# Kernel optimization log

Hardware: AMD Instinct MI355X
Metric: run time of the kernel (lower is better)

The kernel has to match this reference:

```python
import jax, jax.numpy as jnp
import numpy as np

B, P, V = 8, 16, 32
N_TH1 = 20
N_TH2 = 2 * (N_TH1 - 1) + 1
NPC, NNS, NOUT = 16384, 8192, 8192


def make_directions(n_th1):
    n_th2 = 2 * (n_th1 - 1) + 1
    th1 = np.linspace(-np.pi / 2, np.pi / 2, n_th1)
    th2 = np.linspace(-np.pi, np.pi, n_th2)
    c1, s1 = np.cos(th1), np.sin(th1)
    c2, s2 = np.cos(th2), np.sin(th2)
    ds = []
    for i in range(1, n_th1 - 1):
        for j in range(n_th2 - 1):
            ds.append([c1[i] * c2[j], c1[i] * s2[j], s1[i]])
    ds.append([c1[0] * c2[0], c1[0] * s2[0], s1[0]])
    ds.append([c1[-1] * c2[0], c1[-1] * s2[0], s1[-1]])
    return np.asarray(ds, np.float32)

DIRS = jnp.asarray(make_directions(N_TH1))
D = DIRS.shape[0]  # (n_th1-2)*(n_th2-1)+2 = 686


def _spt(dirs, verts, smooth, trans):
    # dirs [B,P,N,3], verts [B,P,V,3] (centered), trans [B,P,1,3]
    z = jnp.einsum('bpvc,bpnc->bpvn', verts, dirs)          # [B,P,V,N]
    zm = jnp.maximum(z, 0.0)
    pe = smooth[:, :, None, None]                            # [B,P,1,1]
    maxz = jnp.clip(jnp.max(z, axis=2, keepdims=True), 1e-30, 1e30)
    k = 1.0 / maxz                                           # [B,P,1,N]
    zmk = jnp.clip(zm * k, 1e-30, 1e30)                      # tiny floor keeps pow grads finite
    sum_zm_p = jnp.sum(zmk ** pe, axis=2, keepdims=True)     # [B,P,1,N]
    h = sum_zm_p ** (1.0 / pe)                               # normalized support value
    s = jnp.clip(h, 1e-30, 1e30)
    dhdz = jnp.clip((zmk / s) ** (pe - 1.0), 1e-30, 1e30)    # [B,P,V,N]
    surf = jnp.einsum('bpvn,bpvc->bpnc', dhdz, verts) + trans
    h_out = jnp.clip(h / k, -1e30, 1e30).transpose(0, 1, 3, 2)  # [B,P,N,1]
    return h_out, surf


def _distance(verts, smooth, trans, pts, normal_filter=None):
    # pts [B,P,N,3]: per-part query points in global coords
    local = pts - trans
    nrm = jnp.sqrt(jnp.clip(jnp.sum(local * local, -1, keepdims=True), 1e-40, 1e40))
    d = local / nrm                                          # unit directions [B,P,N,3]
    h, surf = _spt(d, verts, smooth, trans)
    dist = nrm - h                                           # signed distance to support plane
    if normal_filter is not None:
        dist = jnp.where(normal_filter, 100.0, dist)
    return dist, surf, d


def _overlap(verts, smooth, trans):
    t = trans[:, :, 0, :]                                    # [B,P,3]
    diff = t[:, None, :, :] - t[:, :, None, :]               # [B,i,j,3] = t_j - t_i
    dn = jnp.sqrt(jnp.clip(jnp.sum(diff * diff, -1, keepdims=True), 1e-20, 1e20))
    eyem = jnp.eye(t.shape[1], dtype=t.dtype)[None, :, :, None]
    safe = jnp.array([1.0, 0.0, 0.0], dtype=t.dtype)
    d = diff / dn * (1.0 - eyem) + eyem * safe               # safe diagonal direction
    h, _ = _spt(d, verts, smooth, trans)                     # [B,P,P,1] support of part i toward j
    sep = dn - h - jnp.swapaxes(h, 1, 2)                     # center gap minus both supports
    return jax.nn.relu(-sep) * (1.0 - eyem)


def _forward(vertices, smoothness, pointcloud, nearsurf, out):
    mean_v = jnp.mean(vertices, axis=2, keepdims=True)       # [B,P,1,3]
    local_v = vertices - mean_v
    x = jnp.broadcast_to(DIRS[None, None], (B, P, D, 3))
    h, _ = _spt(x, local_v, smoothness, mean_v)              # [B,P,D,1]
    overlap = _overlap(local_v, smoothness, mean_v)
    pc = jnp.broadcast_to(pointcloud[:, None], (B, P, NPC, 3))
    distance, _, _ = _distance(local_v, smoothness, mean_v, pc)
    scale = jnp.clip(jnp.max(h, axis=2, keepdims=True), 1e-10, 10.0)  # [B,P,1,1]
    _, surf_pts, normals = _distance(local_v, smoothness, mean_v, x * scale + mean_v)
    surf_points = surf_pts.reshape(B, P * D, 3)
    sp2 = jnp.broadcast_to(surf_points[:, None], (B, P, P * D, 3))
    local_trans = jnp.transpose(mean_v, (0, 2, 1, 3)) - mean_v        # [B,P,P,3]
    nf = jnp.einsum('bijc,bidc->bijd', local_trans, normals)          # [B,P,P,D]
    normal_filter = nf.reshape(B, P, P * D)[..., None] < 0
    surf_distance, _, _ = _distance(local_v, smoothness, mean_v, sp2, normal_filter=normal_filter)
    sd = surf_distance.reshape(B, P, P, D, 1)
    df = 100.0 * jnp.eye(P, dtype=sd.dtype)[None, :, :, None, None]
    sd = jnp.where(df > 0, df, sd)                           # mask self-distance
    surf_distance = sd.reshape(B, P, P * D, 1)
    ns = jnp.broadcast_to(nearsurf[:, None], (B, P, NNS, 3))
    nearsurf_dist, _, _ = _distance(local_v, smoothness, mean_v, ns)
    op = jnp.broadcast_to(out[:, None], (B, P, NOUT, 3))
    out_dist, _, _ = _distance(local_v, smoothness, mean_v, op)
    return overlap, distance, x, surf_distance, surf_points, nearsurf_dist, out_dist


def setup_inputs() -> dict:
    key = jax.random.key(0)
    k1, k2, k3, k4, k5, k6 = jax.random.split(key, 6)
    centers = jax.random.uniform(k1, (B, P, 1, 3), minval=-1.0, maxval=1.0)
    vertices = centers + 0.3 * jax.random.normal(k2, (B, P, V, 3))
    smoothness = 2.5 + 7.5 * jax.random.uniform(k3, (B, P))
    pointcloud = jax.random.uniform(k4, (B, NPC, 3), minval=-1.5, maxval=1.5)
    nearsurf = jax.random.uniform(k5, (B, NNS, 3), minval=-1.5, maxval=1.5)
    out = jax.random.uniform(k6, (B, NOUT, 3), minval=-2.0, maxval=2.0)
    return {"vertices": vertices, "smoothness": smoothness, "pointcloud": pointcloud,
            "nearsurf": nearsurf, "out": out}


def reference(vertices, smoothness, pointcloud, nearsurf, out):
    return _forward(vertices, smoothness, pointcloud, nearsurf, out)
```

## Files before the change

kernel.cpp:

```cpp
#include <hip/hip_runtime.h>
#include <math.h>

#define PP 16
#define VV 32
#define DD 686

__device__ __forceinline__ float clampf(float x, float lo, float hi) {
    return fminf(fmaxf(x, lo), hi);
}
__device__ __forceinline__ double clampd(double x, double lo, double hi) {
    return fmin(fmax(x, lo), hi);
}
__device__ __forceinline__ float fexp2(float x) { return __builtin_amdgcn_exp2f(x); }
__device__ __forceinline__ float flog2(float x) { return __builtin_amdgcn_logf(x); }
__device__ __forceinline__ float frcp (float x) { return __builtin_amdgcn_rcpf(x); }
__device__ __forceinline__ float frsq (float x) { return __builtin_amdgcn_rsqf(x); }

__device__ __forceinline__ float spt_support_f(const float* __restrict__ sv, float pe, float inv_pe,
                                               float dx, float dy, float dz)
{
    float z[VV];
    float maxz = -1e38f;
#pragma unroll
    for (int k = 0; k < VV; ++k) {
        float zz = sv[3*k+0]*dx + sv[3*k+1]*dy + sv[3*k+2]*dz;
        z[k] = zz;
        maxz = fmaxf(maxz, zz);
    }
    maxz = clampf(maxz, 1e-30f, 1e30f);
    float kk = frcp(maxz);
    float sum = 0.0f;
#pragma unroll
    for (int k = 0; k < VV; ++k) {
        float zm = clampf(fmaxf(z[k], 0.0f) * kk, 1e-30f, 1e30f);
        sum += fexp2(pe * flog2(zm));
    }
    float h = fexp2(flog2(sum) * inv_pe);
    return clampf(h * maxz, -1e30f, 1e30f);
}

__global__ void k_dirs(float* __restrict__ dirs)
{
    int idx = blockIdx.x * blockDim.x + threadIdx.x;
    if (idx >= DD) return;
    int i, j;
    if (idx < 684)      { i = idx / 38 + 1; j = idx - (idx / 38) * 38; }
    else if (idx == 684){ i = 0;  j = 0; }
    else                { i = 19; j = 0; }
    const double pi = 3.14159265358979323846;
    double th1 = -pi * 0.5 + (double)i * (pi / 19.0);
    double th2 = -pi       + (double)j * (pi / 19.0);
    dirs[3*idx+0] = (float)(cos(th1) * cos(th2));
    dirs[3*idx+1] = (float)(cos(th1) * sin(th2));
    dirs[3*idx+2] = (float)(sin(th1));
}

__global__ void k_prep(const float* __restrict__ verts, const float* __restrict__ smooth,
                       double* __restrict__ dmean, float* __restrict__ fmean,
                       float* __restrict__ flocal, float* __restrict__ fpe,
                       float* __restrict__ finvpe, int BP)
{
    int bp = blockIdx.x * blockDim.x + threadIdx.x;
    if (bp >= BP) return;
    const float* vv = verts + (size_t)bp * VV * 3;
    double sx = 0.0, sy = 0.0, sz = 0.0;
#pragma unroll
    for (int k = 0; k < VV; ++k) {
        sx += (double)vv[3*k+0];
        sy += (double)vv[3*k+1];
        sz += (double)vv[3*k+2];
    }
    double mx = sx / 32.0, my = sy / 32.0, mz = sz / 32.0;
    dmean[3*bp+0] = mx; dmean[3*bp+1] = my; dmean[3*bp+2] = mz;
    fmean[3*bp+0] = (float)mx; fmean[3*bp+1] = (float)my; fmean[3*bp+2] = (float)mz;
    float* lv = flocal + (size_t)bp * VV * 3;
#pragma unroll
    for (int k = 0; k < VV; ++k) {
        lv[3*k+0] = (float)((double)vv[3*k+0] - mx);
        lv[3*k+1] = (float)((double)vv[3*k+1] - my);
        lv[3*k+2] = (float)((double)vv[3*k+2] - mz);
    }
    float pe = smooth[bp];
    fpe[bp] = pe;
    finvpe[bp] = 1.0f / pe;
}

__global__ void __launch_bounds__(256) k_scale_x(
        const float* __restrict__ dirs, const float* __restrict__ flocal,
        const float* __restrict__ fpe, const float* __restrict__ finvpe,
        double* __restrict__ dscale, float* __restrict__ fscale,
        float* __restrict__ out2)
{
    int bp = blockIdx.x;
    __shared__ float sv[VV*3];
    __shared__ float red[4];
    int tid = threadIdx.x;
    if (tid < VV*3) sv[tid] = flocal[(size_t)bp*VV*3 + tid];
    __syncthreads();
    float pe = fpe[bp], ipe = finvpe[bp];
    float m = -1e38f;
    for (int dd = tid; dd < DD; dd += 256) {
        float dxf = dirs[3*dd+0], dyf = dirs[3*dd+1], dzf = dirs[3*dd+2];
        float hs = spt_support_f(sv, pe, ipe, dxf, dyf, dzf);
        m = fmaxf(m, hs);
        float* xp = out2 + ((size_t)bp * DD + dd) * 3;
        xp[0] = dxf; xp[1] = dyf; xp[2] = dzf;
    }
#pragma unroll
    for (int o = 32; o > 0; o >>= 1) m = fmaxf(m, __shfl_down(m, o));
    if ((tid & 63) == 0) red[tid >> 6] = m;
    __syncthreads();
    if (tid == 0) {
        m = fmaxf(fmaxf(red[0], red[1]), fmaxf(red[2], red[3]));
        m = clampf(m, 1e-10f, 10.0f);
        fscale[bp] = m;
        dscale[bp] = (double)m;
    }
}

__global__ void __launch_bounds__(256) k_surfpts(
        const float* __restrict__ dirs, const float* __restrict__ flocal,
        const float* __restrict__ fmean, const float* __restrict__ fpe,
        const float* __restrict__ finvpe, const float* __restrict__ fscale,
        float* __restrict__ fsurf, float* __restrict__ out4)
{
    int bp = blockIdx.x;
    __shared__ float sv[VV*3];
    int tid = threadIdx.x;
    if (tid < VV*3) sv[tid] = flocal[(size_t)bp*VV*3 + tid];
    __syncthreads();
    float pe = fpe[bp], ipe = finvpe[bp];
    float sc = fscale[bp];
    float m0 = fmean[3*bp+0], m1 = fmean[3*bp+1], m2 = fmean[3*bp+2];
    for (int dd = tid; dd < DD; dd += 256) {
        float xd = dirs[3*dd+0], yd = dirs[3*dd+1], zd = dirs[3*dd+2];
        float lx = (xd * sc + m0) - m0;
        float ly = (yd * sc + m1) - m1;
        float lz = (zd * sc + m2) - m2;
        float n2 = clampf(lx*lx + ly*ly + lz*lz, 1e-40f, 1e40f);
        float invr = frsq(n2);
        float dx = lx * invr, dy = ly * invr, dz = lz * invr;

        float l2z[VV];
        float maxz = -1e38f;
        float zz[VV];
#pragma unroll
        for (int k = 0; k < VV; ++k) {
            float z = sv[3*k+0]*dx + sv[3*k+1]*dy + sv[3*k+2]*dz;
            zz[k] = z;
            maxz = fmaxf(maxz, z);
        }
        maxz = clampf(maxz, 1e-30f, 1e30f);
        float kk = frcp(maxz);
        float sum = 0.0f;
#pragma unroll
        for (int k = 0; k < VV; ++k) {
            float zm = clampf(fmaxf(zz[k], 0.0f) * kk, 1e-30f, 1e30f);
            float l2 = flog2(zm);
            l2z[k] = l2;
            sum += fexp2(pe * l2);
        }
        float l2sum = flog2(sum);
        float h = fexp2(l2sum * ipe);
        float s = clampf(h, 1e-30f, 1e30f);
        float l2s = flog2(s);
        float pem1 = pe - 1.0f;
        float sxx = 0.f, syy = 0.f, szz2 = 0.f;
#pragma unroll
        for (int k = 0; k < VV; ++k) {
            float dh = clampf(fexp2(pem1 * (l2z[k] - l2s)), 1e-30f, 1e30f);
            sxx += dh * sv[3*k+0];
            syy += dh * sv[3*k+1];
            szz2 += dh * sv[3*k+2];
        }
        sxx += m0; syy += m1; szz2 += m2;
        float* spp = fsurf + ((size_t)bp * DD + dd) * 3;
        spp[0] = sxx; spp[1] = syy; spp[2] = szz2;
        float* op = out4 + ((size_t)bp * DD + dd) * 3;
        op[0] = sxx; op[1] = syy; op[2] = szz2;
    }
}

__global__ void __launch_bounds__(256) k_overlap(
        const float* __restrict__ flocal, const double* __restrict__ dmean,
        const float* __restrict__ fpe, const float* __restrict__ finvpe,
        float* __restrict__ out0)
{
    int b = blockIdx.x;
    __shared__ float  sv[PP*VV*3];
    __shared__ double smd[PP*3];
    __shared__ float  spe[PP];
    __shared__ float  sipe[PP];
    __shared__ float  sh[PP*PP];
    int tid = threadIdx.x;
    for (int t = tid; t < PP*VV*3; t += 256) sv[t] = flocal[(size_t)b*PP*VV*3 + t];
    if (tid < PP*3) smd[tid]  = dmean[(size_t)b*PP*3 + tid];
    if (tid < PP)  { spe[tid] = fpe[b*PP + tid]; sipe[tid] = finvpe[b*PP + tid]; }
    __syncthreads();
    int i = tid >> 4, j = tid & 15;
    double tx = smd[3*j+0] - smd[3*i+0];
    double ty = smd[3*j+1] - smd[3*i+1];
    double tz = smd[3*j+2] - smd[3*i+2];
    double dn2 = clampd(tx*tx + ty*ty + tz*tz, 1e-20, 1e20);
    double dn = sqrt(dn2);
    float dx, dy, dz;
    if (i == j) { dx = 1.0f; dy = 0.0f; dz = 0.0f; }
    else        { dx = (float)(tx/dn); dy = (float)(ty/dn); dz = (float)(tz/dn); }
    sh[tid] = spt_support_f(&sv[i*VV*3], spe[i], sipe[i], dx, dy, dz);
    __syncthreads();
    double sep = dn - (double)sh[i*16 + j] - (double)sh[j*16 + i];
    double ov = (i == j) ? 0.0 : fmax(-sep, 0.0);
    out0[(size_t)b*PP*PP + tid] = (float)ov;
}

__global__ void __launch_bounds__(256) k_dist(
        const float* __restrict__ pts, int N,
        const float* __restrict__ flocal, const float* __restrict__ fmean,
        const float* __restrict__ fpe, const float* __restrict__ finvpe,
        float* __restrict__ outp)
{
    int bp = blockIdx.x;
    int b  = bp >> 4;
    __shared__ float sv[VV*3];
    int tid = threadIdx.x;
    if (tid < VV*3) sv[tid] = flocal[(size_t)bp*VV*3 + tid];
    __syncthreads();
    float pe = fpe[bp], ipe = finvpe[bp];
    float m0 = fmean[3*bp+0], m1 = fmean[3*bp+1], m2 = fmean[3*bp+2];
    int n = blockIdx.y * 256 + tid;
    if (n >= N) return;
    const float* pp = pts + ((size_t)b * N + n) * 3;
    float lx = pp[0] - m0;
    float ly = pp[1] - m1;
    float lz = pp[2] - m2;
    float n2 = clampf(lx*lx + ly*ly + lz*lz, 1e-40f, 1e40f);
    float invr = frsq(n2);
    float nrm = n2 * invr;
    float dx = lx * invr, dy = ly * invr, dz = lz * invr;
    float hs = spt_support_f(sv, pe, ipe, dx, dy, dz);
    outp[(size_t)bp * N + n] = nrm - hs;
}

__global__ void __launch_bounds__(256) k_surfdist(
        const float* __restrict__ fsurf, const float* __restrict__ dirs,
        const float* __restrict__ flocal, const double* __restrict__ dmean,
        const float* __restrict__ fmean,
        const float* __restrict__ fpe, const float* __restrict__ finvpe,
        const double* __restrict__ dscale,
        float* __restrict__ out3)
{
    int bp = blockIdx.x;
    int b  = bp >> 4;
    int i  = bp & 15;
    __shared__ float sv[VV*3];
    int tid = threadIdx.x;
    if (tid < VV*3) sv[tid] = flocal[(size_t)bp*VV*3 + tid];
    __syncthreads();
    float pe = fpe[bp], ipe = finvpe[bp];
    double sc = dscale[bp];
    double mi0 = dmean[3*bp+0], mi1 = dmean[3*bp+1], mi2 = dmean[3*bp+2];
    int q = blockIdx.y * 256 + tid;
    if (q >= PP*DD) return;
    int j  = q / DD;
    int dd = q - j * DD;
    double xd = (double)dirs[3*dd+0], yd = (double)dirs[3*dd+1], zd = (double)dirs[3*dd+2];
    double nlx = (xd * sc + mi0) - mi0;
    double nly = (yd * sc + mi1) - mi1;
    double nlz = (zd * sc + mi2) - mi2;
    double nn2 = clampd(nlx*nlx + nly*nly + nlz*nlz, 1e-40, 1e40);
    double nnr = sqrt(nn2);
    const double* mj = dmean + (size_t)(b*PP + j) * 3;
    double tx = mj[0] - mi0, ty = mj[1] - mi1, tz = mj[2] - mi2;
    double nf = (tx*nlx + ty*nly + tz*nlz) / nnr;
    float dist;
    if (i == j || nf < 0.0) {
        dist = 100.0f;
    } else {
        float fm0 = fmean[3*bp+0], fm1 = fmean[3*bp+1], fm2 = fmean[3*bp+2];
        const float* sp = fsurf + ((size_t)b * PP * DD + q) * 3;
        float lx = sp[0] - fm0;
        float ly = sp[1] - fm1;
        float lz = sp[2] - fm2;
        float n2 = clampf(lx*lx + ly*ly + lz*lz, 1e-40f, 1e40f);
        float invr = frsq(n2);
        float nrm = n2 * invr;
        float dx = lx * invr, dy = ly * invr, dz = lz * invr;
        float hs = spt_support_f(sv, pe, ipe, dx, dy, dz);
        dist = nrm - hs;
    }
    out3[(size_t)bp * PP * DD + q] = dist;
}

extern "C" void kernel_launch(void* const* d_in, const int* in_sizes, int n_in,
                              void* d_out, int out_size, void* d_ws, size_t ws_size,
                              hipStream_t stream)
{
    const float* verts  = nullptr;
    const float* smooth = nullptr;
    const float* pcb    = nullptr;
    const float* nsb    = nullptr;
    const float* ob     = nullptr;
    const float* dirsin = nullptr;
    int Bv = 8, BP = 128, NPCv = 16384, NNSv = 8192, NOUTv = 8192;

    {
        int si = 0;
        for (int i = 1; i < n_in; ++i) if (in_sizes[i] < in_sizes[si]) si = i;
        int bp = in_sizes[si];
        bool ok = (bp > 0) && (bp % PP == 0);
        int rem[8]; int nrem = 0;
        const float* vcand = nullptr; const float* dcand = nullptr;
        if (ok) {
            for (int i = 0; i < n_in && i < 8; ++i) {
                if (i == si) continue;
                if (!vcand && in_sizes[i] == bp * VV * 3) { vcand = (const float*)d_in[i]; continue; }
                if (!dcand && in_sizes[i] == DD * 3)      { dcand = (const float*)d_in[i]; continue; }
                rem[nrem++] = i;
            }
        }
        if (ok && vcand && nrem == 3) {
            int pci = rem[0];
            for (int r = 1; r < 3; ++r) if (in_sizes[rem[r]] > in_sizes[pci]) pci = rem[r];
            int oth[2]; int no = 0;
            for (int r = 0; r < 3; ++r) if (rem[r] != pci) oth[no++] = rem[r];
            int B = bp / PP;
            int npc = in_sizes[pci] / (3 * B);
            int nns = in_sizes[oth[0]] / (3 * B);
            int nou = in_sizes[oth[1]] / (3 * B);
            if (npc > 0 && nns > 0 && nou > 0) {
                smooth = (const float*)d_in[si];
                verts  = vcand;
                dirsin = dcand;
                pcb    = (const float*)d_in[pci];
                nsb    = (const float*)d_in[oth[0]];
                ob     = (const float*)d_in[oth[1]];
                Bv = B; BP = bp; NPCv = npc; NNSv = nns; NOUTv = nou;
            }
        }
        if (!verts) {
            verts  = (const float*)d_in[0];
            smooth = (const float*)d_in[1];
            pcb    = (const float*)d_in[2];
            nsb    = (const float*)d_in[3];
            ob     = (const float*)d_in[4];
            Bv = 8; BP = 128; NPCv = 16384; NNSv = 8192; NOUTv = 8192;
        }
    }

    double* dmean  = (double*)d_ws;
    double* dscale = dmean + 3*(size_t)BP;
    float*  fdirs  = (float*)(dscale + BP);
    float*  fmean  = fdirs + DD*3;
    float*  fpe    = fmean + 3*(size_t)BP;
    float*  finvpe = fpe + BP;
    float*  fscale = finvpe + BP;
    float*  flocal = fscale + BP;
    float*  fsurf  = flocal + 96*(size_t)BP;

    float* out = (float*)d_out;
    size_t o0 = 0;
    size_t o1 = o0 + (size_t)Bv*PP*PP;
    size_t o2 = o1 + (size_t)BP*NPCv;
    size_t o3 = o2 + (size_t)BP*DD*3;
    size_t o4 = o3 + (size_t)BP*PP*DD;
    size_t o5 = o4 + (size_t)BP*DD*3;
    size_t o6 = o5 + (size_t)BP*NNSv;

    const float* dirs = dirsin ? dirsin : fdirs;
    if (!dirsin) k_dirs<<<dim3(3), 256, 0, stream>>>(fdirs);
    k_prep<<<dim3((BP + 127)/128), 128, 0, stream>>>(verts, smooth, dmean, fmean, flocal,
                                                     fpe, finvpe, BP);
    k_scale_x<<<dim3(BP), 256, 0, stream>>>(dirs, flocal, fpe, finvpe, dscale, fscale, out + o2);
    k_surfpts<<<dim3(BP), 256, 0, stream>>>(dirs, flocal, fmean, fpe, finvpe, fscale,
                                            fsurf, out + o4);
    k_overlap<<<dim3(Bv), 256, 0, stream>>>(flocal, dmean, fpe, finvpe, out + o0);
    k_dist<<<dim3(BP, (NPCv + 255)/256), 256, 0, stream>>>(pcb, NPCv, flocal, fmean, fpe, finvpe, out + o1);
    k_dist<<<dim3(BP, (NNSv + 255)/256), 256, 0, stream>>>(nsb, NNSv, flocal, fmean, fpe, finvpe, out + o5);
    k_dist<<<dim3(BP, (NOUTv + 255)/256), 256, 0, stream>>>(ob, NOUTv, flocal, fmean, fpe, finvpe, out + o6);
    k_surfdist<<<dim3(BP, (PP*DD + 255)/256), 256, 0, stream>>>(fsurf, dirs, flocal, dmean, fmean,
                                                                fpe, finvpe, dscale, out + o3);
}
```

Baseline: 160.2 us.

## Drop max-normalization in support function, fuse shape kernels and distance launches

```diff
diff --git a/kernel.cpp b/kernel.cpp
--- a/kernel.cpp
+++ b/kernel.cpp
@@ -13,30 +13,20 @@
 }
 __device__ __forceinline__ float fexp2(float x) { return __builtin_amdgcn_exp2f(x); }
 __device__ __forceinline__ float flog2(float x) { return __builtin_amdgcn_logf(x); }
-__device__ __forceinline__ float frcp (float x) { return __builtin_amdgcn_rcpf(x); }
 __device__ __forceinline__ float frsq (float x) { return __builtin_amdgcn_rsqf(x); }
 
-__device__ __forceinline__ float spt_support_f(const float* __restrict__ sv, float pe, float inv_pe,
-                                               float dx, float dy, float dz)
-{
-    float z[VV];
-    float maxz = -1e38f;
+__device__ __forceinline__ float spt_h(const float* __restrict__ sv, float pe, float inv_pe,
+                                       float dx, float dy, float dz)
+{
+    float ss[4] = {0.f, 0.f, 0.f, 0.f};
 #pragma unroll
     for (int k = 0; k < VV; ++k) {
-        float zz = sv[3*k+0]*dx + sv[3*k+1]*dy + sv[3*k+2]*dz;
-        z[k] = zz;
-        maxz = fmaxf(maxz, zz);
-    }
-    maxz = clampf(maxz, 1e-30f, 1e30f);
-    float kk = frcp(maxz);
-    float sum = 0.0f;
-#pragma unroll
-    for (int k = 0; k < VV; ++k) {
-        float zm = clampf(fmaxf(z[k], 0.0f) * kk, 1e-30f, 1e30f);
-        sum += fexp2(pe * flog2(zm));
-    }
-    float h = fexp2(flog2(sum) * inv_pe);
-    return clampf(h * maxz, -1e30f, 1e30f);
+        float z = sv[3*k+0]*dx + sv[3*k+1]*dy + sv[3*k+2]*dz;
+        z = fmaxf(z, 1e-30f);
+        ss[k & 3] += fexp2(pe * flog2(z));
+    }
+    float sum = (ss[0] + ss[1]) + (ss[2] + ss[3]);
+    return fexp2(flog2(sum) * inv_pe);
 }
 
 __global__ void k_dirs(float* __restrict__ dirs)
@@ -85,11 +75,12 @@
     finvpe[bp] = 1.0f / pe;
 }
 
-__global__ void __launch_bounds__(256) k_scale_x(
+__global__ void __launch_bounds__(256) k_shape(
         const float* __restrict__ dirs, const float* __restrict__ flocal,
+        const float* __restrict__ fmean,
         const float* __restrict__ fpe, const float* __restrict__ finvpe,
-        double* __restrict__ dscale, float* __restrict__ fscale,
-        float* __restrict__ out2)
+        double* __restrict__ dscale,
+        float* __restrict__ out2, float* __restrict__ fsurf, float* __restrict__ out4)
 {
     int bp = blockIdx.x;
     __shared__ float sv[VV*3];
@@ -98,13 +89,28 @@
     if (tid < VV*3) sv[tid] = flocal[(size_t)bp*VV*3 + tid];
     __syncthreads();
     float pe = fpe[bp], ipe = finvpe[bp];
+    float m0 = fmean[3*bp+0], m1 = fmean[3*bp+1], m2 = fmean[3*bp+2];
+
+    float l2h_reg[3];
     float m = -1e38f;
-    for (int dd = tid; dd < DD; dd += 256) {
-        float dxf = dirs[3*dd+0], dyf = dirs[3*dd+1], dzf = dirs[3*dd+2];
-        float hs = spt_support_f(sv, pe, ipe, dxf, dyf, dzf);
-        m = fmaxf(m, hs);
+#pragma unroll
+    for (int it = 0; it < 3; ++it) {
+        int dd = tid + 256*it;
+        if (dd >= DD) break;
+        float dx = dirs[3*dd+0], dy = dirs[3*dd+1], dz = dirs[3*dd+2];
+        float ss[4] = {0.f,0.f,0.f,0.f};
+#pragma unroll
+        for (int k = 0; k < VV; ++k) {
+            float z = sv[3*k+0]*dx + sv[3*k+1]*dy + sv[3*k+2]*dz;
+            z = fmaxf(z, 1e-30f);
+            ss[k & 3] += fexp2(pe * flog2(z));
+        }
+        float sum = (ss[0]+ss[1]) + (ss[2]+ss[3]);
+        float l2h = flog2(sum) * ipe;
+        l2h_reg[it] = l2h;
+        m = fmaxf(m, fexp2(l2h));
         float* xp = out2 + ((size_t)bp * DD + dd) * 3;
-        xp[0] = dxf; xp[1] = dyf; xp[2] = dzf;
+        xp[0] = dx; xp[1] = dy; xp[2] = dz;
     }
 #pragma unroll
     for (int o = 32; o > 0; o >>= 1) m = fmaxf(m, __shfl_down(m, o));
@@ -112,72 +118,30 @@
     __syncthreads();
     if (tid == 0) {
         m = fmaxf(fmaxf(red[0], red[1]), fmaxf(red[2], red[3]));
-        m = clampf(m, 1e-10f, 10.0f);
-        fscale[bp] = m;
-        dscale[bp] = (double)m;
-    }
-}
-
-__global__ void __launch_bounds__(256) k_surfpts(
-        const float* __restrict__ dirs, const float* __restrict__ flocal,
-        const float* __restrict__ fmean, const float* __restrict__ fpe,
-        const float* __restrict__ finvpe, const float* __restrict__ fscale,
-        float* __restrict__ fsurf, float* __restrict__ out4)
-{
-    int bp = blockIdx.x;
-    __shared__ float sv[VV*3];
-    int tid = threadIdx.x;
-    if (tid < VV*3) sv[tid] = flocal[(size_t)bp*VV*3 + tid];
-    __syncthreads();
-    float pe = fpe[bp], ipe = finvpe[bp];
-    float sc = fscale[bp];
-    float m0 = fmean[3*bp+0], m1 = fmean[3*bp+1], m2 = fmean[3*bp+2];
-    for (int dd = tid; dd < DD; dd += 256) {
-        float xd = dirs[3*dd+0], yd = dirs[3*dd+1], zd = dirs[3*dd+2];
-        float lx = (xd * sc + m0) - m0;
-        float ly = (yd * sc + m1) - m1;
-        float lz = (zd * sc + m2) - m2;
-        float n2 = clampf(lx*lx + ly*ly + lz*lz, 1e-40f, 1e40f);
-        float invr = frsq(n2);
-        float dx = lx * invr, dy = ly * invr, dz = lz * invr;
-
-        float l2z[VV];
-        float maxz = -1e38f;
-        float zz[VV];
+        dscale[bp] = (double)clampf(m, 1e-10f, 10.0f);
+    }
+
+    float pem1 = pe - 1.0f;
+#pragma unroll
+    for (int it = 0; it < 3; ++it) {
+        int dd = tid + 256*it;
+        if (dd >= DD) break;
+        float dx = dirs[3*dd+0], dy = dirs[3*dd+1], dz = dirs[3*dd+2];
+        float l2h = l2h_reg[it];
+        float sxx = 0.f, syy = 0.f, szz = 0.f;
 #pragma unroll
         for (int k = 0; k < VV; ++k) {
-            float z = sv[3*k+0]*dx + sv[3*k+1]*dy + sv[3*k+2]*dz;
-            zz[k] = z;
-            maxz = fmaxf(maxz, z);
-        }
-        maxz = clampf(maxz, 1e-30f, 1e30f);
-        float kk = frcp(maxz);
-        float sum = 0.0f;
-#pragma unroll
-        for (int k = 0; k < VV; ++k) {
-            float zm = clampf(fmaxf(zz[k], 0.0f) * kk, 1e-30f, 1e30f);
-            float l2 = flog2(zm);
-            l2z[k] = l2;
-            sum += fexp2(pe * l2);
-        }
-        float l2sum = flog2(sum);
-        float h = fexp2(l2sum * ipe);
-        float s = clampf(h, 1e-30f, 1e30f);
-        float l2s = flog2(s);
-        float pem1 = pe - 1.0f;
-        float sxx = 0.f, syy = 0.f, szz2 = 0.f;
-#pragma unroll
-        for (int k = 0; k < VV; ++k) {
-            float dh = clampf(fexp2(pem1 * (l2z[k] - l2s)), 1e-30f, 1e30f);
-            sxx += dh * sv[3*k+0];
-            syy += dh * sv[3*k+1];
-            szz2 += dh * sv[3*k+2];
-        }
-        sxx += m0; syy += m1; szz2 += m2;
+            float vx = sv[3*k+0], vy = sv[3*k+1], vz = sv[3*k+2];
+            float z = vx*dx + vy*dy + vz*dz;
+            z = fmaxf(z, 1e-30f);
+            float dh = fexp2(pem1 * (flog2(z) - l2h));
+            sxx += dh * vx; syy += dh * vy; szz += dh * vz;
+        }
+        sxx += m0; syy += m1; szz += m2;
         float* spp = fsurf + ((size_t)bp * DD + dd) * 3;
-        spp[0] = sxx; spp[1] = syy; spp[2] = szz2;
+        spp[0] = sxx; spp[1] = syy; spp[2] = szz;
         float* op = out4 + ((size_t)bp * DD + dd) * 3;
-        op[0] = sxx; op[1] = syy; op[2] = szz2;
+        op[0] = sxx; op[1] = syy; op[2] = szz;
     }
 }
 
@@ -206,18 +170,20 @@
     float dx, dy, dz;
     if (i == j) { dx = 1.0f; dy = 0.0f; dz = 0.0f; }
     else        { dx = (float)(tx/dn); dy = (float)(ty/dn); dz = (float)(tz/dn); }
-    sh[tid] = spt_support_f(&sv[i*VV*3], spe[i], sipe[i], dx, dy, dz);
+    sh[tid] = spt_h(&sv[i*VV*3], spe[i], sipe[i], dx, dy, dz);
     __syncthreads();
     double sep = dn - (double)sh[i*16 + j] - (double)sh[j*16 + i];
     double ov = (i == j) ? 0.0 : fmax(-sep, 0.0);
     out0[(size_t)b*PP*PP + tid] = (float)ov;
 }
 
-__global__ void __launch_bounds__(256) k_dist(
-        const float* __restrict__ pts, int N,
+__global__ void __launch_bounds__(256) k_dist_all(
+        const float* __restrict__ pc, int NPCv, int cPC,
+        const float* __restrict__ ns, int NNSv, int cNS,
+        const float* __restrict__ ob, int NOUTv,
         const float* __restrict__ flocal, const float* __restrict__ fmean,
         const float* __restrict__ fpe, const float* __restrict__ finvpe,
-        float* __restrict__ outp)
+        float* __restrict__ out1, float* __restrict__ out5, float* __restrict__ out6)
 {
     int bp = blockIdx.x;
     int b  = bp >> 4;
@@ -227,7 +193,13 @@
     __syncthreads();
     float pe = fpe[bp], ipe = finvpe[bp];
     float m0 = fmean[3*bp+0], m1 = fmean[3*bp+1], m2 = fmean[3*bp+2];
-    int n = blockIdx.y * 256 + tid;
+
+    int y = blockIdx.y;
+    const float* pts; int N; float* outp;
+    if (y < cPC)            { pts = pc; N = NPCv;  outp = out1; }
+    else if ((y -= cPC) < cNS) { pts = ns; N = NNSv;  outp = out5; }
+    else                    { y -= cNS; pts = ob; N = NOUTv; outp = out6; }
+    int n = y * 256 + tid;
     if (n >= N) return;
     const float* pp = pts + ((size_t)b * N + n) * 3;
     float lx = pp[0] - m0;
@@ -236,8 +208,7 @@
     float n2 = clampf(lx*lx + ly*ly + lz*lz, 1e-40f, 1e40f);
     float invr = frsq(n2);
     float nrm = n2 * invr;
-    float dx = lx * invr, dy = ly * invr, dz = lz * invr;
-    float hs = spt_support_f(sv, pe, ipe, dx, dy, dz);
+    float hs = spt_h(sv, pe, ipe, lx, ly, lz) * invr;
     outp[(size_t)bp * N + n] = nrm - hs;
 }
 
@@ -284,8 +255,7 @@
         float n2 = clampf(lx*lx + ly*ly + lz*lz, 1e-40f, 1e40f);
         float invr = frsq(n2);
         float nrm = n2 * invr;
-        float dx = lx * invr, dy = ly * invr, dz = lz * invr;
-        float hs = spt_support_f(sv, pe, ipe, dx, dy, dz);
+        float hs = spt_h(sv, pe, ipe, lx, ly, lz) * invr;
         dist = nrm - hs;
     }
     out3[(size_t)bp * PP * DD + q] = dist;
@@ -353,8 +323,7 @@
     float*  fmean  = fdirs + DD*3;
     float*  fpe    = fmean + 3*(size_t)BP;
     float*  finvpe = fpe + BP;
-    float*  fscale = finvpe + BP;
-    float*  flocal = fscale + BP;
+    float*  flocal = finvpe + BP;
     float*  fsurf  = flocal + 96*(size_t)BP;
 
     float* out = (float*)d_out;
@@ -370,13 +339,13 @@
     if (!dirsin) k_dirs<<<dim3(3), 256, 0, stream>>>(fdirs);
     k_prep<<<dim3((BP + 127)/128), 128, 0, stream>>>(verts, smooth, dmean, fmean, flocal,
                                                      fpe, finvpe, BP);
-    k_scale_x<<<dim3(BP), 256, 0, stream>>>(dirs, flocal, fpe, finvpe, dscale, fscale, out + o2);
-    k_surfpts<<<dim3(BP), 256, 0, stream>>>(dirs, flocal, fmean, fpe, finvpe, fscale,
-                                            fsurf, out + o4);
+    k_shape<<<dim3(BP), 256, 0, stream>>>(dirs, flocal, fmean, fpe, finvpe, dscale,
+                                          out + o2, fsurf, out + o4);
     k_overlap<<<dim3(Bv), 256, 0, stream>>>(flocal, dmean, fpe, finvpe, out + o0);
-    k_dist<<<dim3(BP, (NPCv + 255)/256), 256, 0, stream>>>(pcb, NPCv, flocal, fmean, fpe, finvpe, out + o1);
-    k_dist<<<dim3(BP, (NNSv + 255)/256), 256, 0, stream>>>(nsb, NNSv, flocal, fmean, fpe, finvpe, out + o5);
-    k_dist<<<dim3(BP, (NOUTv + 255)/256), 256, 0, stream>>>(ob, NOUTv, flocal, fmean, fpe, finvpe, out + o6);
+    int cPC = (NPCv + 255)/256, cNS = (NNSv + 255)/256, cOU = (NOUTv + 255)/256;
+    k_dist_all<<<dim3(BP, cPC + cNS + cOU), 256, 0, stream>>>(
+        pcb, NPCv, cPC, nsb, NNSv, cNS, ob, NOUTv,
+        flocal, fmean, fpe, finvpe, out + o1, out + o5, out + o6);
     k_surfdist<<<dim3(BP, (PP*DD + 255)/256), 256, 0, stream>>>(fsurf, dirs, flocal, dmean, fmean,
                                                                 fpe, finvpe, dscale, out + o3);
 }
```

New measurement: 145.3 us. 1.1x faster.
